# Kernel tuning notes

Hardware: AMD Instinct MI355X
Metric: run time of the kernel (lower is better)

Reference implementation:

```python
import jax, jax.numpy as jnp
import numpy as np

K = 2            # top-k experts
TEMP = 1.0       # temperature
LN_EPS = 1e-5

def setup_inputs() -> dict:
    key = jax.random.key(0)
    B, S, D, E = 4, 4096, 2048, 64
    k0, k1, k2, k3 = jax.random.split(key, 4)
    x = jax.random.normal(k0, (B, S, D), dtype=jnp.float32)
    Wg = jax.random.normal(k1, (E, D), dtype=jnp.float32) * 0.02       # base_gate weight [out,in]
    gamma = jnp.ones((D,), jnp.float32)                                 # LayerNorm weight
    beta = jnp.zeros((D,), jnp.float32)                                 # LayerNorm bias
    W1 = jax.random.normal(k2, (D // 2, D), dtype=jnp.float32) * 0.02   # diff_pred linear1
    W2 = jax.random.normal(k3, (1, D // 2), dtype=jnp.float32) * 0.02   # diff_pred linear2
    return {"x": x, "Wg": Wg, "gamma": gamma, "beta": beta, "W1": W1, "W2": W2}

def reference(x, Wg, gamma, beta, W1, W2):
    # base expert logits: [B,S,E]
    logits = jnp.einsum('bsd,ed->bse', x, Wg)
    # difficulty predictor: LN -> Linear -> GELU -> Linear -> sigmoid, [B,S,1]
    mu = jnp.mean(x, axis=-1, keepdims=True)
    var = jnp.var(x, axis=-1, keepdims=True)
    h = (x - mu) * jax.lax.rsqrt(var + LN_EPS) * gamma + beta
    h1 = jax.nn.gelu(jnp.einsum('bsd,hd->bsh', h, W1), approximate=False)
    diff = jax.nn.sigmoid(jnp.einsum('bsh,oh->bso', h1, W2))
    # modulate + temperature (eval mode: no jitter / mask_drop)
    logits = logits / (1.0 + diff) * (1.0 / TEMP)
    probs_soft = jax.nn.softmax(logits, axis=-1)
    # top-k selection
    _, idx = jax.lax.top_k(logits, K)                    # [B,S,K]
    hard_any = jnp.max(jax.nn.one_hot(idx, logits.shape[-1], dtype=probs_soft.dtype), axis=2)  # [B,S,E]
    probs_st = hard_any - probs_soft + probs_soft        # faithful to source (no detach)
    scores = jnp.take_along_axis(probs_st, idx, axis=-1)  # [B,S,K]
    scores = scores / jnp.maximum(jnp.sum(scores, axis=-1, keepdims=True), 1e-9)
    importance = jax.lax.stop_gradient(jnp.mean(probs_soft, axis=(0, 1)))  # [E]
    load = jax.lax.stop_gradient(jnp.mean(hard_any, axis=(0, 1)))          # [E]
    return (idx, scores, probs_soft, importance, load)
```

## Files before the change

### kernel.cpp

```cpp
#include <hip/hip_runtime.h>
#include <math.h>

#define BS_TOK 16384
#define DIM    2048
#define NEXP   64
#define DHID   1024
#define GKS    4
#define KSL    (DIM / GKS)

typedef __attribute__((ext_vector_type(8))) _Float16 f16x8;
typedef __attribute__((ext_vector_type(4))) float    f32x4;

#define GLOBAL_AS const __attribute__((address_space(1))) void*
#define LDS_AS    __attribute__((address_space(3))) void*

__device__ __forceinline__ float gelu_f(float x) {
  return 0.5f * x * (1.0f + erff(x * 0.70710678118654752440f));
}

__global__ __launch_bounds__(256) void lnw1_kernel(const float* __restrict__ X,
                                                   const float* __restrict__ gamma,
                                                   const float* __restrict__ beta,
                                                   _Float16* __restrict__ H,
                                                   const float* __restrict__ W1,
                                                   _Float16* __restrict__ W1h) {
  const int tid = threadIdx.x;
  if (blockIdx.x >= BS_TOK / 4) {
    const int i = ((blockIdx.x - BS_TOK / 4) * 256 + tid) * 8;
    const float4 a = *(const float4*)(W1 + i);
    const float4 b = *(const float4*)(W1 + i + 4);
    f16x8 o;
    o[0] = (_Float16)a.x; o[1] = (_Float16)a.y; o[2] = (_Float16)a.z; o[3] = (_Float16)a.w;
    o[4] = (_Float16)b.x; o[5] = (_Float16)b.y; o[6] = (_Float16)b.z; o[7] = (_Float16)b.w;
    *(f16x8*)(W1h + i) = o;
    return;
  }
  const int w    = tid >> 6, lane = tid & 63;
  const int t    = blockIdx.x * 4 + w;
  const float* xr = X + (size_t)t * DIM;
  float4 xv[8];
#pragma unroll
  for (int j = 0; j < 4; ++j) {
    const int c0 = (j * 64 + lane) * 8;
    xv[j * 2]     = *(const float4*)(xr + c0);
    xv[j * 2 + 1] = *(const float4*)(xr + c0 + 4);
  }
  float s = 0.f, q = 0.f;
#pragma unroll
  for (int j = 0; j < 8; ++j) {
    s += (xv[j].x + xv[j].y) + (xv[j].z + xv[j].w);
    q += (xv[j].x * xv[j].x + xv[j].y * xv[j].y) + (xv[j].z * xv[j].z + xv[j].w * xv[j].w);
  }
#pragma unroll
  for (int off = 32; off > 0; off >>= 1) {
    s += __shfl_xor(s, off);
    q += __shfl_xor(q, off);
  }
  const float mu  = s * (1.0f / DIM);
  const float var = q * (1.0f / DIM) - mu * mu;
  const float rs  = rsqrtf(var + 1e-5f);
#pragma unroll
  for (int j = 0; j < 4; ++j) {
    const int c0 = (j * 64 + lane) * 8;
    const float4 g0 = *(const float4*)(gamma + c0);
    const float4 g1 = *(const float4*)(gamma + c0 + 4);
    const float4 b0 = *(const float4*)(beta + c0);
    const float4 b1 = *(const float4*)(beta + c0 + 4);
    const float4 a = xv[j * 2], b = xv[j * 2 + 1];
    f16x8 h;
    h[0] = (_Float16)((a.x - mu) * rs * g0.x + b0.x);
    h[1] = (_Float16)((a.y - mu) * rs * g0.y + b0.y);
    h[2] = (_Float16)((a.z - mu) * rs * g0.z + b0.z);
    h[3] = (_Float16)((a.w - mu) * rs * g0.w + b0.w);
    h[4] = (_Float16)((b.x - mu) * rs * g1.x + b1.x);
    h[5] = (_Float16)((b.y - mu) * rs * g1.y + b1.y);
    h[6] = (_Float16)((b.z - mu) * rs * g1.z + b1.z);
    h[7] = (_Float16)((b.w - mu) * rs * g1.w + b1.w);
    *(f16x8*)(H + (size_t)t * DIM + c0) = h;
  }
}

#define GT_M 256
#define PX   260
#define PW   68
__global__ __launch_bounds__(256) void gate_kernel(const float* __restrict__ X,
                                                   const float* __restrict__ Wg,
                                                   float* __restrict__ logitsP) {
  __shared__ float sX[16][PX];
  __shared__ float sW[16][PW];
  const int tid  = threadIdx.x;
  const int m0   = blockIdx.x * GT_M;
  const int k0   = blockIdx.y * KSL;
  const int srow = tid >> 2;
  const int skq  = tid & 3;
  const int ty   = tid >> 3;
  const int tx   = tid & 7;
  const float* xb = X  + (size_t)(m0 + srow) * DIM + k0 + skq * 4;
  const float* wb = Wg + (size_t)srow * DIM + k0 + skq * 4;
  float acc[8][8] = {};
  float4 rx[4], rw;
#pragma unroll
  for (int g = 0; g < 4; ++g) rx[g] = *(const float4*)(xb + (size_t)(g * 64) * DIM);
  rw = *(const float4*)wb;
  for (int kt = 0; kt < KSL; kt += 16) {
    __syncthreads();
#pragma unroll
    for (int g = 0; g < 4; ++g) {
      sX[skq * 4 + 0][srow + g * 64] = rx[g].x;
      sX[skq * 4 + 1][srow + g * 64] = rx[g].y;
      sX[skq * 4 + 2][srow + g * 64] = rx[g].z;
      sX[skq * 4 + 3][srow + g * 64] = rx[g].w;
    }
    sW[skq * 4 + 0][srow] = rw.x;
    sW[skq * 4 + 1][srow] = rw.y;
    sW[skq * 4 + 2][srow] = rw.z;
    sW[skq * 4 + 3][srow] = rw.w;
    const int ktn = (kt + 16 < KSL) ? kt + 16 : 0;
#pragma unroll
    for (int g = 0; g < 4; ++g) rx[g] = *(const float4*)(xb + (size_t)(g * 64) * DIM + ktn);
    rw = *(const float4*)(wb + ktn);
    __syncthreads();
#pragma unroll
    for (int k = 0; k < 16; ++k) {
      const float4 a0 = *(const float4*)&sX[k][ty * 8];
      const float4 a1 = *(const float4*)&sX[k][ty * 8 + 4];
      const float4 b0 = *(const float4*)&sW[k][tx * 8];
      const float4 b1 = *(const float4*)&sW[k][tx * 8 + 4];
      const float av[8] = {a0.x, a0.y, a0.z, a0.w, a1.x, a1.y, a1.z, a1.w};
      const float bv[8] = {b0.x, b0.y, b0.z, b0.w, b1.x, b1.y, b1.z, b1.w};
#pragma unroll
      for (int i = 0; i < 8; ++i)
#pragma unroll
        for (int j = 0; j < 8; ++j) acc[i][j] += av[i] * bv[j];
    }
  }
  float* op = logitsP + (size_t)blockIdx.y * ((size_t)BS_TOK * NEXP)
            + (size_t)(m0 + ty * 8) * NEXP + tx * 8;
#pragma unroll
  for (int i = 0; i < 8; ++i) {
    float4 o0, o1;
    o0.x = acc[i][0]; o0.y = acc[i][1]; o0.z = acc[i][2]; o0.w = acc[i][3];
    o1.x = acc[i][4]; o1.y = acc[i][5]; o1.z = acc[i][6]; o1.w = acc[i][7];
    *(float4*)(op + (size_t)i * NEXP)     = o0;
    *(float4*)(op + (size_t)i * NEXP + 4) = o1;
  }
}

#define G2BM 256
#define G2BN 256
#define G2BK 32
#define G2NT (DIM / G2BK)

__global__ __launch_bounds__(512, 2) void g2_kernel(const _Float16* __restrict__ H,
                                                    const _Float16* __restrict__ W1h,
                                                    const float* __restrict__ W2,
                                                    float* __restrict__ diffz) {
  __shared__ __align__(16) _Float16 sA[3][G2BM * G2BK];
  __shared__ __align__(16) _Float16 sB[3][G2BN * G2BK];
  const int bid = blockIdx.x;
  const int xcd = bid & 7;
  const int loc = bid >> 3;
  const int m0  = (xcd * 8 + (loc >> 2)) * G2BM;
  const int n0  = (loc & 3) * G2BN;
  const int tid  = threadIdx.x;
  const int lane = tid & 63;
  const int w    = tid >> 6;
  const int wr   = w >> 2, wc = w & 3;
  const int col  = lane & 15, quad = lane >> 4;
  const int sq   = (quad ^ (col & 3)) * 8;
  const int srow4 = tid >> 2;
  const int ksw   = (tid & 3) ^ (srow4 & 3);
  const _Float16* gA = H   + (size_t)(m0 + srow4) * DIM + ksw * 8;
  const _Float16* gB = W1h + (size_t)(n0 + srow4) * DIM + ksw * 8;
  f32x4 acc[8][4] = {};
#define G2_STAGE(bf_, kt_) do {                                                                             \
    __builtin_amdgcn_global_load_lds((GLOBAL_AS)(gA + (kt_)), (LDS_AS)(sA[bf_] + tid * 8), 16, 0, 0);        \
    __builtin_amdgcn_global_load_lds((GLOBAL_AS)(gA + (size_t)128 * DIM + (kt_)), (LDS_AS)(sA[bf_] + 4096 + tid * 8), 16, 0, 0); \
    __builtin_amdgcn_global_load_lds((GLOBAL_AS)(gB + (kt_)), (LDS_AS)(sB[bf_] + tid * 8), 16, 0, 0);        \
    __builtin_amdgcn_global_load_lds((GLOBAL_AS)(gB + (size_t)128 * DIM + (kt_)), (LDS_AS)(sB[bf_] + 4096 + tid * 8), 16, 0, 0); \
  } while (0)
  G2_STAGE(0, 0);
  G2_STAGE(1, G2BK);
  asm volatile("s_waitcnt vmcnt(4)" ::: "memory");
  __builtin_amdgcn_s_barrier();
  int cur = 0;
  for (int t = 0; t < G2NT; ++t) {
    const _Float16* A = sA[cur];
    const _Float16* B = sB[cur];
    const int nb = (cur >= 1) ? cur - 1 : 2;
    if (t + 2 < G2NT) G2_STAGE(nb, (t + 2) * G2BK);
    f16x8 af[4], bfr[4];
#pragma unroll
    for (int ni = 0; ni < 4; ++ni)
      bfr[ni] = *(const f16x8*)(B + (wc * 64 + ni * 16 + col) * G2BK + sq);
#pragma unroll
    for (int mi = 0; mi < 4; ++mi)
      af[mi] = *(const f16x8*)(A + (wr * 128 + mi * 16 + col) * G2BK + sq);
    __builtin_amdgcn_s_barrier();
    __builtin_amdgcn_s_setprio(1);
#pragma unroll
    for (int mi = 0; mi < 4; ++mi)
#pragma unroll
      for (int ni = 0; ni < 4; ++ni)
        acc[mi][ni] = __builtin_amdgcn_mfma_f32_16x16x32_f16(af[mi], bfr[ni], acc[mi][ni], 0, 0, 0);
    __builtin_amdgcn_s_setprio(0);
    __builtin_amdgcn_s_barrier();
#pragma unroll
    for (int mi = 0; mi < 4; ++mi)
      af[mi] = *(const f16x8*)(A + (wr * 128 + (mi + 4) * 16 + col) * G2BK + sq);
    __builtin_amdgcn_s_barrier();
    __builtin_amdgcn_s_setprio(1);
#pragma unroll
    for (int mi = 0; mi < 4; ++mi)
#pragma unroll
      for (int ni = 0; ni < 4; ++ni)
        acc[mi + 4][ni] = __builtin_amdgcn_mfma_f32_16x16x32_f16(af[mi], bfr[ni], acc[mi + 4][ni], 0, 0, 0);
    __builtin_amdgcn_s_setprio(0);
    if (t + 2 < G2NT) asm volatile("s_waitcnt vmcnt(4) lgkmcnt(0)" ::: "memory");
    else              asm volatile("s_waitcnt vmcnt(0) lgkmcnt(0)" ::: "memory");
    __builtin_amdgcn_sched_barrier(0);
    __builtin_amdgcn_s_barrier();
    cur = (cur == 2) ? 0 : cur + 1;
  }
#undef G2_STAGE
  float w2v[4];
#pragma unroll
  for (int ni = 0; ni < 4; ++ni) w2v[ni] = W2[n0 + wc * 64 + ni * 16 + col];
#pragma unroll
  for (int mi = 0; mi < 8; ++mi) {
#pragma unroll
    for (int reg = 0; reg < 4; ++reg) {
      float v = 0.f;
#pragma unroll
      for (int ni = 0; ni < 4; ++ni) v += gelu_f(acc[mi][ni][reg]) * w2v[ni];
      v += __shfl_xor(v, 1);
      v += __shfl_xor(v, 2);
      v += __shfl_xor(v, 4);
      v += __shfl_xor(v, 8);
      if (col == 0)
        atomicAdd(diffz + m0 + wr * 128 + mi * 16 + quad * 4 + reg, v);
    }
  }
}

__global__ __launch_bounds__(256) void finalize_kernel(const float* __restrict__ logitsP,
                                                       const float* __restrict__ diffz,
                                                       float* __restrict__ out_idx,
                                                       float* __restrict__ out_scores,
                                                       float* __restrict__ out_probs,
                                                       float* __restrict__ accs,
                                                       float* __restrict__ out_imp,
                                                       float* __restrict__ out_load) {
  const int tid  = threadIdx.x;
  const int w    = tid >> 6, lane = tid & 63;
  const size_t PS = (size_t)BS_TOK * NEXP;
  float acc_imp = 0.f, acc_load = 0.f;
  for (int it = 0; it < 8; ++it) {
    const int t    = blockIdx.x * 32 + it * 4 + w;
    const float* lp = logitsP + (size_t)t * NEXP + lane;
    const float L  = ((lp[0] + lp[PS]) + lp[2 * PS]) + lp[3 * PS];
    const float z  = diffz[t];
    const float d  = 1.0f / (1.0f + expf(-z));
    const float l  = L / (1.0f + d);
    float m = l;
#pragma unroll
    for (int off = 32; off > 0; off >>= 1) m = fmaxf(m, __shfl_xor(m, off));
    float p = expf(l - m);
    float s = p;
#pragma unroll
    for (int off = 32; off > 0; off >>= 1) s += __shfl_xor(s, off);
    p /= s;
    float v = l; int bi = lane;
#pragma unroll
    for (int off = 32; off > 0; off >>= 1) {
      const float ov = __shfl_xor(v, off);
      const int   oi = __shfl_xor(bi, off);
      if (ov > v || (ov == v && oi < bi)) { v = ov; bi = oi; }
    }
    const int i1 = bi;
    float v2 = (lane == i1) ? -INFINITY : l;
    int bi2 = lane;
#pragma unroll
    for (int off = 32; off > 0; off >>= 1) {
      const float ov = __shfl_xor(v2, off);
      const int   oi = __shfl_xor(bi2, off);
      if (ov > v2 || (ov == v2 && oi < bi2)) { v2 = ov; bi2 = oi; }
    }
    const int i2 = bi2;
    const float p1 = __shfl(p, i1);
    const float p2 = __shfl(p, i2);
    const float s1 = (1.0f - p1) + p1;
    const float s2 = (1.0f - p2) + p2;
    const float den = fmaxf(s1 + s2, 1e-9f);
    if (lane == 0) {
      out_idx[t * 2]        = (float)i1;
      out_idx[t * 2 + 1]    = (float)i2;
      out_scores[t * 2]     = s1 / den;
      out_scores[t * 2 + 1] = s2 / den;
    }
    out_probs[(size_t)t * NEXP + lane] = p;
    acc_imp  += p;
    acc_load += (lane == i1 || lane == i2) ? 1.0f : 0.0f;
  }
  __shared__ float s_imp[256];
  __shared__ float s_hard[256];
  s_imp[tid]  = acc_imp;
  s_hard[tid] = acc_load;
  __syncthreads();
  if (tid < 64) {
    const float si = s_imp[tid] + s_imp[64 + tid] + s_imp[128 + tid] + s_imp[192 + tid];
    const float sl = s_hard[tid] + s_hard[64 + tid] + s_hard[128 + tid] + s_hard[192 + tid];
    atomicAdd(accs + tid, si);
    atomicAdd(accs + 64 + tid, sl);
    __threadfence();
  }
  __shared__ int lastf;
  __syncthreads();
  if (tid == 0) {
    unsigned* cnt = (unsigned*)(accs + 128);
    lastf = (atomicAdd(cnt, 1u) == (unsigned)(BS_TOK / 32) - 1u);
  }
  __syncthreads();
  if (lastf && tid < 128) {
    const float v = atomicAdd(accs + tid, 0.0f);
    const float inv = 1.0f / 16384.0f;
    if (tid < 64) out_imp[tid]       = v * inv;
    else          out_load[tid - 64] = v * inv;
  }
}

extern "C" void kernel_launch(void* const* d_in, const int* in_sizes, int n_in,
                              void* d_out, int out_size, void* d_ws, size_t ws_size,
                              hipStream_t stream) {
  (void)in_sizes; (void)n_in; (void)out_size; (void)ws_size;
  const float* X     = (const float*)d_in[0];
  const float* Wg    = (const float*)d_in[1];
  const float* gamma = (const float*)d_in[2];
  const float* beta  = (const float*)d_in[3];
  const float* W1    = (const float*)d_in[4];
  const float* W2    = (const float*)d_in[5];
  float* out = (float*)d_out;

  char* ws = (char*)d_ws;
  _Float16* H       = (_Float16*)(ws);
  _Float16* W1h     = (_Float16*)(ws + 67108864ull);
  float*    logitsP = (float*)  (ws + 71303168ull);
  float*    diffz   = (float*)  (ws + 88080384ull);
  float*    accs    = (float*)  (ws + 88145920ull);

  float* out_idx    = out;
  float* out_scores = out + 32768;
  float* out_probs  = out + 65536;
  float* out_imp    = out + 1114112;
  float* out_load   = out + 1114176;

  hipMemsetAsync(diffz, 0, 66560ull, stream);
  gate_kernel<<<dim3(BS_TOK / GT_M, GKS), 256, 0, stream>>>(X, Wg, logitsP);
  lnw1_kernel<<<BS_TOK / 4 + (DHID * DIM) / (256 * 8), 256, 0, stream>>>(X, gamma, beta, H, W1, W1h);
  g2_kernel<<<(DHID / G2BN) * (BS_TOK / G2BM), 512, 0, stream>>>(H, W1h, W2, diffz);
  finalize_kernel<<<BS_TOK / 32, 256, 0, stream>>>(logitsP, diffz, out_idx, out_scores,
                                                   out_probs, accs, out_imp, out_load);
}
```

Measured before the change: 391.5 us.

## Shrink g2 GEMM tile to 128x128 with single-buffered LDS and higher occupancy

After: 375.7 us. 1.04x faster.

```diff
diff --git a/kernel.cpp b/kernel.cpp
--- a/kernel.cpp
+++ b/kernel.cpp
@@ -146,88 +146,61 @@
   }
 }
 
-#define G2BM 256
-#define G2BN 256
+#define G2BM 128
+#define G2BN 128
 #define G2BK 32
 #define G2NT (DIM / G2BK)
 
-__global__ __launch_bounds__(512, 2) void g2_kernel(const _Float16* __restrict__ H,
+__global__ __launch_bounds__(256, 4) void g2_kernel(const _Float16* __restrict__ H,
                                                     const _Float16* __restrict__ W1h,
                                                     const float* __restrict__ W2,
                                                     float* __restrict__ diffz) {
-  __shared__ __align__(16) _Float16 sA[3][G2BM * G2BK];
-  __shared__ __align__(16) _Float16 sB[3][G2BN * G2BK];
+  __shared__ __align__(16) _Float16 sA[G2BM * G2BK];
+  __shared__ __align__(16) _Float16 sB[G2BN * G2BK];
   const int bid = blockIdx.x;
   const int xcd = bid & 7;
   const int loc = bid >> 3;
-  const int m0  = (xcd * 8 + (loc >> 2)) * G2BM;
-  const int n0  = (loc & 3) * G2BN;
+  const int m0  = (xcd * 16 + (loc >> 3)) * G2BM;
+  const int n0  = (loc & 7) * G2BN;
   const int tid  = threadIdx.x;
   const int lane = tid & 63;
   const int w    = tid >> 6;
-  const int wr   = w >> 2, wc = w & 3;
+  const int wr   = w >> 1, wc = w & 1;
   const int col  = lane & 15, quad = lane >> 4;
-  const int sq   = (quad ^ (col & 3)) * 8;
-  const int srow4 = tid >> 2;
-  const int ksw   = (tid & 3) ^ (srow4 & 3);
-  const _Float16* gA = H   + (size_t)(m0 + srow4) * DIM + ksw * 8;
-  const _Float16* gB = W1h + (size_t)(n0 + srow4) * DIM + ksw * 8;
-  f32x4 acc[8][4] = {};
-#define G2_STAGE(bf_, kt_) do {                                                                             \
-    __builtin_amdgcn_global_load_lds((GLOBAL_AS)(gA + (kt_)), (LDS_AS)(sA[bf_] + tid * 8), 16, 0, 0);        \
-    __builtin_amdgcn_global_load_lds((GLOBAL_AS)(gA + (size_t)128 * DIM + (kt_)), (LDS_AS)(sA[bf_] + 4096 + tid * 8), 16, 0, 0); \
-    __builtin_amdgcn_global_load_lds((GLOBAL_AS)(gB + (kt_)), (LDS_AS)(sB[bf_] + tid * 8), 16, 0, 0);        \
-    __builtin_amdgcn_global_load_lds((GLOBAL_AS)(gB + (size_t)128 * DIM + (kt_)), (LDS_AS)(sB[bf_] + 4096 + tid * 8), 16, 0, 0); \
-  } while (0)
-  G2_STAGE(0, 0);
-  G2_STAGE(1, G2BK);
-  asm volatile("s_waitcnt vmcnt(4)" ::: "memory");
-  __builtin_amdgcn_s_barrier();
-  int cur = 0;
+  const int sq   = (quad ^ ((col >> 1) & 3)) * 8;
+  const int srow = tid >> 2;
+  const int ksw  = (tid & 3) ^ ((tid >> 3) & 3);
+  const _Float16* gA = H   + (size_t)(m0 + srow) * DIM + ksw * 8;
+  const _Float16* gB = W1h + (size_t)(n0 + srow) * DIM + ksw * 8;
+  f32x4 acc[4][4] = {};
   for (int t = 0; t < G2NT; ++t) {
-    const _Float16* A = sA[cur];
-    const _Float16* B = sB[cur];
-    const int nb = (cur >= 1) ? cur - 1 : 2;
-    if (t + 2 < G2NT) G2_STAGE(nb, (t + 2) * G2BK);
-    f16x8 af[4], bfr[4];
+    const int kt = t * G2BK;
+    __syncthreads();
+    __builtin_amdgcn_global_load_lds((GLOBAL_AS)(gA + kt), (LDS_AS)(sA + tid * 8), 16, 0, 0);
+    __builtin_amdgcn_global_load_lds((GLOBAL_AS)(gA + (size_t)64 * DIM + kt), (LDS_AS)(sA + 2048 + tid * 8), 16, 0, 0);
+    __builtin_amdgcn_global_load_lds((GLOBAL_AS)(gB + kt), (LDS_AS)(sB + tid * 8), 16, 0, 0);
+    __builtin_amdgcn_global_load_lds((GLOBAL_AS)(gB + (size_t)64 * DIM + kt), (LDS_AS)(sB + 2048 + tid * 8), 16, 0, 0);
+    __syncthreads();
+    f16x8 af[4], bf[4];
+#pragma unroll
+    for (int mi = 0; mi < 4; ++mi)
+      af[mi] = *(const f16x8*)(sA + (wr * 64 + mi * 16 + col) * G2BK + sq);
 #pragma unroll
     for (int ni = 0; ni < 4; ++ni)
-      bfr[ni] = *(const f16x8*)(B + (wc * 64 + ni * 16 + col) * G2BK + sq);
+      bf[ni] = *(const f16x8*)(sB + (wc * 64 + ni * 16 + col) * G2BK + sq);
+    __builtin_amdgcn_s_setprio(1);
 #pragma unroll
     for (int mi = 0; mi < 4; ++mi)
-      af[mi] = *(const f16x8*)(A + (wr * 128 + mi * 16 + col) * G2BK + sq);
-    __builtin_amdgcn_s_barrier();
-    __builtin_amdgcn_s_setprio(1);
-#pragma unroll
-    for (int mi = 0; mi < 4; ++mi)
 #pragma unroll
       for (int ni = 0; ni < 4; ++ni)
-        acc[mi][ni] = __builtin_amdgcn_mfma_f32_16x16x32_f16(af[mi], bfr[ni], acc[mi][ni], 0, 0, 0);
+        acc[mi][ni] = __builtin_amdgcn_mfma_f32_16x16x32_f16(af[mi], bf[ni], acc[mi][ni], 0, 0, 0);
     __builtin_amdgcn_s_setprio(0);
-    __builtin_amdgcn_s_barrier();
-#pragma unroll
-    for (int mi = 0; mi < 4; ++mi)
-      af[mi] = *(const f16x8*)(A + (wr * 128 + (mi + 4) * 16 + col) * G2BK + sq);
-    __builtin_amdgcn_s_barrier();
-    __builtin_amdgcn_s_setprio(1);
-#pragma unroll
-    for (int mi = 0; mi < 4; ++mi)
-#pragma unroll
-      for (int ni = 0; ni < 4; ++ni)
-        acc[mi + 4][ni] = __builtin_amdgcn_mfma_f32_16x16x32_f16(af[mi], bfr[ni], acc[mi + 4][ni], 0, 0, 0);
-    __builtin_amdgcn_s_setprio(0);
-    if (t + 2 < G2NT) asm volatile("s_waitcnt vmcnt(4) lgkmcnt(0)" ::: "memory");
-    else              asm volatile("s_waitcnt vmcnt(0) lgkmcnt(0)" ::: "memory");
-    __builtin_amdgcn_sched_barrier(0);
-    __builtin_amdgcn_s_barrier();
-    cur = (cur == 2) ? 0 : cur + 1;
-  }
-#undef G2_STAGE
+  }
   float w2v[4];
 #pragma unroll
   for (int ni = 0; ni < 4; ++ni) w2v[ni] = W2[n0 + wc * 64 + ni * 16 + col];
 #pragma unroll
-  for (int mi = 0; mi < 8; ++mi) {
+  for (int mi = 0; mi < 4; ++mi) {
 #pragma unroll
     for (int reg = 0; reg < 4; ++reg) {
       float v = 0.f;
@@ -238,7 +211,7 @@
       v += __shfl_xor(v, 4);
       v += __shfl_xor(v, 8);
       if (col == 0)
-        atomicAdd(diffz + m0 + wr * 128 + mi * 16 + quad * 4 + reg, v);
+        atomicAdd(diffz + m0 + wr * 64 + mi * 16 + quad * 4 + reg, v);
     }
   }
 }
@@ -357,7 +330,7 @@
   hipMemsetAsync(diffz, 0, 66560ull, stream);
   gate_kernel<<<dim3(BS_TOK / GT_M, GKS), 256, 0, stream>>>(X, Wg, logitsP);
   lnw1_kernel<<<BS_TOK / 4 + (DHID * DIM) / (256 * 8), 256, 0, stream>>>(X, gamma, beta, H, W1, W1h);
-  g2_kernel<<<(DHID / G2BN) * (BS_TOK / G2BM), 512, 0, stream>>>(H, W1h, W2, diffz);
+  g2_kernel<<<(DHID / G2BN) * (BS_TOK / G2BM), 256, 0, stream>>>(H, W1h, W2, diffz);
   finalize_kernel<<<BS_TOK / 32, 256, 0, stream>>>(logitsP, diffz, out_idx, out_scores,
                                                    out_probs, accs, out_imp, out_load);
 }
```
